# Performance work log

Hardware: AMD Instinct MI355X
Metric: run time of the kernel (lower is better)

## Reference

```python
import jax, jax.numpy as jnp
import numpy as np

D = 128  # hard-coded hidden dim in MLP_T

def setup_inputs() -> dict:
    key = jax.random.key(0)
    ks = jax.random.split(key, 8)
    N, IN = 16384, 768
    return {
        "x": jax.random.normal(ks[0], (N, IN), dtype=jnp.float32),
        "decay_value": 1,
        "W_token": jax.random.normal(ks[1], (IN, D), dtype=jnp.float32) * (IN ** -0.5),
        "b_token": jax.random.normal(ks[2], (D,), dtype=jnp.float32) * 0.02,
        "W_qkv": jax.random.normal(ks[3], (D, 3 * D), dtype=jnp.float32) * (D ** -0.5),
        "b_qkv": jax.random.normal(ks[4], (3 * D,), dtype=jnp.float32) * 0.02,
        "W_fc": jax.random.normal(ks[5], (D, 1), dtype=jnp.float32) * (D ** -0.5),
        "b_fc": jax.random.normal(ks[6], (1,), dtype=jnp.float32) * 0.02,
    }

def reference(x, decay_value, W_token, b_token, W_qkv, b_qkv, W_fc, b_fc):
    # token projection: [N, in_chan] -> [N, 128]
    h = x @ W_token + b_token
    # qkv: [N, 384] split along feature dim into q, k, v of [N, 128]
    qkv = h @ W_qkv + b_qkv
    q, k, v = qkv[:, :D], qkv[:, D:2 * D], qkv[:, 2 * D:]
    # sigmoid attention (no row normalization); dropout is identity in eval mode
    att_scores = jax.nn.sigmoid(q @ k.T)            # [N, N]
    att = att_scores @ v                            # [N, 128]
    out = att @ W_fc + b_fc                         # [N, 1]
    # GradientReversal is identity in the forward pass
    return out
```

## Files before the change

kernel.cpp:

```cpp
#include <hip/hip_runtime.h>
#include <hip/hip_bf16.h>
#include <stdint.h>

#define N_ROWS 16384

typedef __bf16 bf16x8 __attribute__((ext_vector_type(8)));
typedef float f32x4 __attribute__((ext_vector_type(4)));

#define AS1 __attribute__((address_space(1)))
#define AS3 __attribute__((address_space(3)))

#define OFF_WCS  0u
#define OFF_BC   589824u
#define OFF_QB   591360u
#define OFF_KB   4785664u
#define OFF_WV   8979968u
#define OFF_PART 9045504u

__global__ void prep(const float* __restrict__ Wt, const float* __restrict__ Wq,
                     const float* __restrict__ bt, const float* __restrict__ bq,
                     __bf16* __restrict__ WcS, float* __restrict__ bc) {
    int u = blockIdx.x * 256 + threadIdx.x;
    if (u < 768 * 96) {
        int k = u / 96, n4 = u % 96;
        float s[4] = {0, 0, 0, 0};
        const float* wtp = Wt + k * 128;
        const float* wqp = Wq + n4 * 4;
#pragma unroll 8
        for (int d = 0; d < 128; d++) {
            float a = wtp[d];
            float4 b = *(const float4*)(wqp + d * 384);
            s[0] += a * b.x; s[1] += a * b.y; s[2] += a * b.z; s[3] += a * b.w;
        }
        int kb_ = k >> 6, c = (k >> 3) & 7, k7 = k & 7;
#pragma unroll
        for (int j = 0; j < 4; j++) {
            int n = n4 * 4 + j;
            WcS[n * 768 + kb_ * 64 + ((c ^ (n & 7)) << 3) + k7] = (__bf16)s[j];
        }
    }
    if (u < 384) {
        float s = bq[u];
        for (int d = 0; d < 128; d++) s += bt[d] * Wq[d * 384 + u];
        bc[u] = s;
    }
}

__launch_bounds__(256)
__global__ void gemm_qkv(const float* __restrict__ x, const __bf16* __restrict__ WcS,
                         const float* __restrict__ bc, const float* __restrict__ W_fc,
                         __bf16* __restrict__ qb, __bf16* __restrict__ kb,
                         float* __restrict__ wv) {
    __shared__ float  Asm[64 * 64];
    __shared__ __bf16 Bsm[128 * 64];
    __shared__ float  wred[64];
    const int tid = threadIdx.x, wave = tid >> 6, lane = tid & 63;
    const int n16 = lane & 15, q = lane >> 4;
    const int mh = wave >> 1, nw = wave & 1;
    const int row0 = blockIdx.x * 64;
    const int sp = blockIdx.y;

    const char* aptr[4];
    const char* bptr[4];
    {
        int p = (lane & 15) >> 1, half = lane & 1;
#pragma unroll
        for (int i = 0; i < 4; i++) {
            int ar = row0 + wave * 16 + i * 4 + (lane >> 4);
            aptr[i] = (const char*)x + (size_t)ar * 3072 + ((p ^ (ar & 7)) * 8 + half * 4) * 4;
            int br = sp * 128 + wave * 32 + i * 8 + (lane >> 3);
            bptr[i] = (const char*)WcS + (size_t)br * 1536 + (lane & 7) * 16;
        }
    }
    f32x4 acc[2][4];
#pragma unroll
    for (int mt = 0; mt < 2; mt++)
#pragma unroll
        for (int t = 0; t < 4; t++) acc[mt][t] = (f32x4){0, 0, 0, 0};

    for (int kbi = 0; kbi < 12; kbi++) {
#pragma unroll
        for (int i = 0; i < 4; i++)
            __builtin_amdgcn_global_load_lds((const AS1 void*)(aptr[i] + kbi * 256),
                (AS3 void*)((char*)Asm + wave * 4096 + i * 1024), 16, 0, 0);
#pragma unroll
        for (int i = 0; i < 4; i++)
            __builtin_amdgcn_global_load_lds((const AS1 void*)(bptr[i] + kbi * 128),
                (AS3 void*)((char*)Bsm + wave * 4096 + i * 1024), 16, 0, 0);
        __syncthreads();
#pragma unroll
        for (int ks = 0; ks < 2; ks++) {
            const int swz = ((ks * 4 + q) ^ (n16 & 7)) << 3;
            bf16x8 af[2];
#pragma unroll
            for (int mt = 0; mt < 2; mt++) {
                const float* ap = Asm + (mh * 32 + mt * 16 + n16) * 64 + swz;
                f32x4 a0 = *(const f32x4*)ap;
                f32x4 a1 = *(const f32x4*)(ap + 4);
                bf16x8 t;
                t[0] = (__bf16)a0[0]; t[1] = (__bf16)a0[1]; t[2] = (__bf16)a0[2]; t[3] = (__bf16)a0[3];
                t[4] = (__bf16)a1[0]; t[5] = (__bf16)a1[1]; t[6] = (__bf16)a1[2]; t[7] = (__bf16)a1[3];
                af[mt] = t;
            }
#pragma unroll
            for (int t = 0; t < 4; t++) {
                bf16x8 bf = *(const bf16x8*)(Bsm + (nw * 64 + t * 16 + n16) * 64 + swz);
                acc[0][t] = __builtin_amdgcn_mfma_f32_16x16x32_bf16(af[0], bf, acc[0][t], 0, 0, 0);
                acc[1][t] = __builtin_amdgcn_mfma_f32_16x16x32_bf16(af[1], bf, acc[1][t], 0, 0, 0);
            }
        }
        __syncthreads();
    }

    const int clb = nw * 64 + n16;
    if (sp == 0) {
#pragma unroll
        for (int t = 0; t < 4; t++) {
            int cl = clb + t * 16;
            float bcv = bc[cl];
#pragma unroll
            for (int mt = 0; mt < 2; mt++)
#pragma unroll
                for (int r = 0; r < 4; r++) {
                    int row = row0 + mh * 32 + mt * 16 + q * 4 + r;
                    qb[row * 128 + cl] = (__bf16)((acc[mt][t][r] + bcv) * -1.44269504088896f);
                }
        }
    } else if (sp == 1) {
#pragma unroll
        for (int t = 0; t < 4; t++) {
            int d = clb + t * 16;
            float bcv = bc[128 + d];
#pragma unroll
            for (int mt = 0; mt < 2; mt++)
#pragma unroll
                for (int r = 0; r < 4; r++) {
                    int row = row0 + mh * 32 + mt * 16 + q * 4 + r;
                    kb[row * 128 + (((d >> 3) ^ (row & 15)) << 3) + (d & 7)] = (__bf16)(acc[mt][t][r] + bcv);
                }
        }
    } else {
        float wacc[2][4] = {{0, 0, 0, 0}, {0, 0, 0, 0}};
#pragma unroll
        for (int t = 0; t < 4; t++) {
            int cl = clb + t * 16;
            float bcv = bc[256 + cl];
            float wf = W_fc[cl];
#pragma unroll
            for (int mt = 0; mt < 2; mt++)
#pragma unroll
                for (int r = 0; r < 4; r++) wacc[mt][r] += (acc[mt][t][r] + bcv) * wf;
        }
        float vred[2][4];
#pragma unroll
        for (int mt = 0; mt < 2; mt++)
#pragma unroll
            for (int r = 0; r < 4; r++) {
                float v = wacc[mt][r];
                v += __shfl_xor(v, 1, 64);
                v += __shfl_xor(v, 2, 64);
                v += __shfl_xor(v, 4, 64);
                v += __shfl_xor(v, 8, 64);
                vred[mt][r] = v;
                if (nw == 0 && n16 == 0) wred[mh * 32 + mt * 16 + q * 4 + r] = v;
            }
        __syncthreads();
        if (nw == 1 && n16 == 0) {
#pragma unroll
            for (int mt = 0; mt < 2; mt++)
#pragma unroll
                for (int r = 0; r < 4; r++) {
                    int lr = mh * 32 + mt * 16 + q * 4 + r;
                    wv[row0 + lr] = wred[lr] + vred[mt][r];
                }
        }
    }
}

__launch_bounds__(256, 4)
__global__ void attn(const __bf16* __restrict__ qb, const __bf16* __restrict__ kb,
                     const float* __restrict__ wv, float* __restrict__ partial) {
    __shared__ __bf16 kbuf[4 * 32 * 128];
    const int tid = threadIdx.x;
    const int wave = tid >> 6, lane = tid & 63;
    const int n16 = lane & 15, q = lane >> 4;
    const int bid = blockIdx.x;
    const int sp = bid & 7;
    const int rb = bid >> 3;
    const int row0 = rb * 128 + wave * 32;
    const int jb0 = sp * 2048;

    bf16x8 qf[2][4];
#pragma unroll
    for (int mt = 0; mt < 2; mt++)
#pragma unroll
        for (int ks = 0; ks < 4; ks++)
            qf[mt][ks] = *(const bf16x8*)(qb + (size_t)(row0 + mt * 16 + n16) * 128 + ks * 32 + q * 8);

    float acc[2][4] = {{0}, {0}};

#define ISSUE(c, slot)                                                                  \
    {                                                                                   \
        const char* gsrc = (const char*)kb + (size_t)(jb0 + (c) * 32) * 256 + wave * 2048; \
        char* gdst = (char*)kbuf + (slot) * 8192 + wave * 2048;                          \
        __builtin_amdgcn_global_load_lds((const AS1 void*)(gsrc + lane * 16),            \
                                         (AS3 void*)gdst, 16, 0, 0);                     \
        __builtin_amdgcn_global_load_lds((const AS1 void*)(gsrc + 1024 + lane * 16),     \
                                         (AS3 void*)(gdst + 1024), 16, 0, 0);            \
    }

    ISSUE(0, 0);
    ISSUE(1, 1);

    for (int jc = 0; jc < 64; jc++) {
        const int jn = (jc + 2 < 64) ? jc + 2 : 63;
        ISSUE(jn, (jc + 2) & 3);

        asm volatile("s_waitcnt vmcnt(4)" ::: "memory");
        __builtin_amdgcn_sched_barrier(0);
        __builtin_amdgcn_s_barrier();

        const __bf16* curK = kbuf + (jc & 3) * 4096;
#pragma unroll
        for (int t = 0; t < 2; t++) {
            f32x4 s0 = (f32x4){0, 0, 0, 0}, s1 = (f32x4){0, 0, 0, 0};
#pragma unroll
            for (int ks = 0; ks < 4; ks++) {
                const int chunk = (ks * 4 + q) ^ n16;
                bf16x8 bf = *(const bf16x8*)(curK + (t * 16 + n16) * 128 + chunk * 8);
                s0 = __builtin_amdgcn_mfma_f32_16x16x32_bf16(qf[0][ks], bf, s0, 0, 0, 0);
                s1 = __builtin_amdgcn_mfma_f32_16x16x32_bf16(qf[1][ks], bf, s1, 0, 0, 0);
            }
            const float wval = wv[jb0 + jc * 32 + t * 16 + n16];
#pragma unroll
            for (int r = 0; r < 4; r++) {
                acc[0][r] += __builtin_amdgcn_rcpf(1.0f + __builtin_amdgcn_exp2f(s0[r])) * wval;
                acc[1][r] += __builtin_amdgcn_rcpf(1.0f + __builtin_amdgcn_exp2f(s1[r])) * wval;
            }
        }
    }
#undef ISSUE

#pragma unroll
    for (int mt = 0; mt < 2; mt++)
#pragma unroll
        for (int r = 0; r < 4; r++) {
            float v = acc[mt][r];
            v += __shfl_xor(v, 1, 64);
            v += __shfl_xor(v, 2, 64);
            v += __shfl_xor(v, 4, 64);
            v += __shfl_xor(v, 8, 64);
            if (n16 == 0) partial[sp * N_ROWS + row0 + mt * 16 + q * 4 + r] = v;
        }
}

__global__ void reduce_out(const float* __restrict__ partial, const float* __restrict__ b_fc,
                           float* __restrict__ out) {
    int i = blockIdx.x * 256 + threadIdx.x;
    float v = b_fc[0];
#pragma unroll
    for (int s = 0; s < 8; s++) v += partial[s * N_ROWS + i];
    out[i] = v;
}

extern "C" void kernel_launch(void* const* d_in, const int* in_sizes, int n_in,
                              void* d_out, int out_size, void* d_ws, size_t ws_size,
                              hipStream_t stream) {
    const float* x       = (const float*)d_in[0];
    const float* W_token = (const float*)d_in[2];
    const float* b_token = (const float*)d_in[3];
    const float* W_qkv   = (const float*)d_in[4];
    const float* b_qkv   = (const float*)d_in[5];
    const float* W_fc    = (const float*)d_in[6];
    const float* b_fc    = (const float*)d_in[7];
    float* out = (float*)d_out;
    char* ws = (char*)d_ws;

    __bf16* WcS = (__bf16*)(ws + OFF_WCS);
    float*  bc  = (float*)(ws + OFF_BC);
    __bf16* qb  = (__bf16*)(ws + OFF_QB);
    __bf16* kb  = (__bf16*)(ws + OFF_KB);
    float*  wv  = (float*)(ws + OFF_WV);
    float*  part = (float*)(ws + OFF_PART);

    prep<<<288, 256, 0, stream>>>(W_token, W_qkv, b_token, b_qkv, WcS, bc);
    gemm_qkv<<<dim3(256, 3), 256, 0, stream>>>(x, WcS, bc, W_fc, qb, kb, wv);
    attn<<<1024, 256, 0, stream>>>(qb, kb, wv, part);
    reduce_out<<<64, 256, 0, stream>>>(part, b_fc, out);
}
```

Measured before the change: 203.8 us.

## Software-pipeline sigmoid epilogue behind next MFMA tile and process K chunks in pairs

```diff
diff --git a/kernel.cpp b/kernel.cpp
--- a/kernel.cpp
+++ b/kernel.cpp
@@ -196,50 +196,76 @@
 #pragma unroll
         for (int ks = 0; ks < 4; ks++)
             qf[mt][ks] = *(const bf16x8*)(qb + (size_t)(row0 + mt * 16 + n16) * 128 + ks * 32 + q * 8);
-
-    float acc[2][4] = {{0}, {0}};
-
-#define ISSUE(c, slot)                                                                  \
-    {                                                                                   \
-        const char* gsrc = (const char*)kb + (size_t)(jb0 + (c) * 32) * 256 + wave * 2048; \
-        char* gdst = (char*)kbuf + (slot) * 8192 + wave * 2048;                          \
-        __builtin_amdgcn_global_load_lds((const AS1 void*)(gsrc + lane * 16),            \
-                                         (AS3 void*)gdst, 16, 0, 0);                     \
-        __builtin_amdgcn_global_load_lds((const AS1 void*)(gsrc + 1024 + lane * 16),     \
-                                         (AS3 void*)(gdst + 1024), 16, 0, 0);            \
-    }
+    __builtin_amdgcn_sched_barrier(0);
+
+    auto ISSUE = [&](int c, int slot) {
+        const char* gsrc = (const char*)kb + (size_t)(jb0 + c * 32) * 256 + wave * 2048;
+        char* gdst = (char*)kbuf + slot * 8192 + wave * 2048;
+        __builtin_amdgcn_global_load_lds((const AS1 void*)(gsrc + lane * 16),
+                                         (AS3 void*)gdst, 16, 0, 0);
+        __builtin_amdgcn_global_load_lds((const AS1 void*)(gsrc + 1024 + lane * 16),
+                                         (AS3 void*)(gdst + 1024), 16, 0, 0);
+    };
 
     ISSUE(0, 0);
     ISSUE(1, 1);
 
-    for (int jc = 0; jc < 64; jc++) {
-        const int jn = (jc + 2 < 64) ? jc + 2 : 63;
-        ISSUE(jn, (jc + 2) & 3);
-
-        asm volatile("s_waitcnt vmcnt(4)" ::: "memory");
+    float acc[2][4] = {{0}, {0}};
+    f32x4 ps0 = (f32x4){0, 0, 0, 0}, ps1 = (f32x4){0, 0, 0, 0};
+    float pw = 0.0f;
+
+    const __bf16* kaddr[4];
+#pragma unroll
+    for (int ks = 0; ks < 4; ks++)
+        kaddr[ks] = kbuf + n16 * 128 + (((ks * 4 + q) ^ n16) << 3);
+    const float* wsl = wv + jb0 + n16;
+
+    auto STEP = [&](int off, float wnew) {
+        f32x4 s0 = (f32x4){0, 0, 0, 0}, s1 = (f32x4){0, 0, 0, 0};
+        __builtin_amdgcn_s_setprio(1);
+#pragma unroll
+        for (int ks = 0; ks < 4; ks++) {
+            bf16x8 bf = *(const bf16x8*)(kaddr[ks] + off);
+            s0 = __builtin_amdgcn_mfma_f32_16x16x32_bf16(qf[0][ks], bf, s0, 0, 0, 0);
+            s1 = __builtin_amdgcn_mfma_f32_16x16x32_bf16(qf[1][ks], bf, s1, 0, 0, 0);
+        }
+        __builtin_amdgcn_s_setprio(0);
+#pragma unroll
+        for (int r = 0; r < 4; r++) {
+            acc[0][r] += __builtin_amdgcn_rcpf(1.0f + __builtin_amdgcn_exp2f(ps0[r])) * pw;
+            acc[1][r] += __builtin_amdgcn_rcpf(1.0f + __builtin_amdgcn_exp2f(ps1[r])) * pw;
+        }
+        ps0 = s0; ps1 = s1; pw = wnew;
+    };
+
+    auto PAIR = [&](int p, int sb) {
+        asm volatile("s_waitcnt vmcnt(0)" ::: "memory");
         __builtin_amdgcn_sched_barrier(0);
         __builtin_amdgcn_s_barrier();
-
-        const __bf16* curK = kbuf + (jc & 3) * 4096;
-#pragma unroll
-        for (int t = 0; t < 2; t++) {
-            f32x4 s0 = (f32x4){0, 0, 0, 0}, s1 = (f32x4){0, 0, 0, 0};
-#pragma unroll
-            for (int ks = 0; ks < 4; ks++) {
-                const int chunk = (ks * 4 + q) ^ n16;
-                bf16x8 bf = *(const bf16x8*)(curK + (t * 16 + n16) * 128 + chunk * 8);
-                s0 = __builtin_amdgcn_mfma_f32_16x16x32_bf16(qf[0][ks], bf, s0, 0, 0, 0);
-                s1 = __builtin_amdgcn_mfma_f32_16x16x32_bf16(qf[1][ks], bf, s1, 0, 0, 0);
-            }
-            const float wval = wv[jb0 + jc * 32 + t * 16 + n16];
-#pragma unroll
-            for (int r = 0; r < 4; r++) {
-                acc[0][r] += __builtin_amdgcn_rcpf(1.0f + __builtin_amdgcn_exp2f(s0[r])) * wval;
-                acc[1][r] += __builtin_amdgcn_rcpf(1.0f + __builtin_amdgcn_exp2f(s1[r])) * wval;
-            }
-        }
-    }
-#undef ISSUE
+        const int c2 = (2 * p + 2 < 64) ? 2 * p + 2 : 62;
+        const int c3 = (2 * p + 3 < 64) ? 2 * p + 3 : 63;
+        ISSUE(c2, sb ^ 2);
+        ISSUE(c3, (sb ^ 2) + 1);
+        float w0 = wsl[p * 64];
+        float w1 = wsl[p * 64 + 16];
+        float w2 = wsl[p * 64 + 32];
+        float w3 = wsl[p * 64 + 48];
+        STEP(sb * 4096,        w0);
+        STEP(sb * 4096 + 2048, w1);
+        STEP(sb * 4096 + 4096, w2);
+        STEP(sb * 4096 + 6144, w3);
+    };
+
+    for (int p = 0; p < 32; p += 2) {
+        PAIR(p, 0);
+        PAIR(p + 1, 2);
+    }
+
+#pragma unroll
+    for (int r = 0; r < 4; r++) {
+        acc[0][r] += __builtin_amdgcn_rcpf(1.0f + __builtin_amdgcn_exp2f(ps0[r])) * pw;
+        acc[1][r] += __builtin_amdgcn_rcpf(1.0f + __builtin_amdgcn_exp2f(ps1[r])) * pw;
+    }
 
 #pragma unroll
     for (int mt = 0; mt < 2; mt++)
```

New measurement: 234.4 us. 15.0% more time.

## Software-pipeline sigmoid epilogue against next tile's MFMAs in attention loop

Applied to the files above, without the earlier changes.

```diff
diff --git a/kernel.cpp b/kernel.cpp
--- a/kernel.cpp
+++ b/kernel.cpp
@@ -196,8 +196,7 @@
 #pragma unroll
         for (int ks = 0; ks < 4; ks++)
             qf[mt][ks] = *(const bf16x8*)(qb + (size_t)(row0 + mt * 16 + n16) * 128 + ks * 32 + q * 8);
-
-    float acc[2][4] = {{0}, {0}};
+    __builtin_amdgcn_sched_barrier(0);
 
 #define ISSUE(c, slot)                                                                  \
     {                                                                                   \
@@ -209,37 +208,73 @@
                                          (AS3 void*)(gdst + 1024), 16, 0, 0);            \
     }
 
+    const float* wsl = wv + jb0 + n16;
+    float wnA0 = wsl[0], wnA1 = wsl[16];
+    float wnB0 = 0.0f, wnB1 = 0.0f;
+    __builtin_amdgcn_sched_barrier(0);
     ISSUE(0, 0);
     ISSUE(1, 1);
 
+    float acc[2][4] = {{0}, {0}};
+    f32x4 psE0 = (f32x4){0, 0, 0, 0}, psE1 = (f32x4){0, 0, 0, 0};
+    f32x4 psO0 = (f32x4){0, 0, 0, 0}, psO1 = (f32x4){0, 0, 0, 0};
+    float pw = 0.0f;
+
+    const __bf16* kaddr[4];
+#pragma unroll
+    for (int ks = 0; ks < 4; ks++)
+        kaddr[ks] = kbuf + n16 * 128 + (((ks * 4 + q) ^ n16) << 3);
+
+#define STEP(SW0, SW1, SR0, SR1, OFFB, WCUR)                                            \
+    {                                                                                   \
+        SW0 = (f32x4){0, 0, 0, 0};                                                      \
+        SW1 = (f32x4){0, 0, 0, 0};                                                      \
+        __builtin_amdgcn_s_setprio(1);                                                  \
+        _Pragma("unroll")                                                               \
+        for (int ks = 0; ks < 4; ks++) {                                                \
+            bf16x8 bf = *(const bf16x8*)(kaddr[ks] + (OFFB));                           \
+            SW0 = __builtin_amdgcn_mfma_f32_16x16x32_bf16(qf[0][ks], bf, SW0, 0, 0, 0); \
+            SW1 = __builtin_amdgcn_mfma_f32_16x16x32_bf16(qf[1][ks], bf, SW1, 0, 0, 0); \
+        }                                                                               \
+        __builtin_amdgcn_s_setprio(0);                                                  \
+        _Pragma("unroll")                                                               \
+        for (int r = 0; r < 4; r++) {                                                   \
+            acc[0][r] += __builtin_amdgcn_rcpf(1.0f + __builtin_amdgcn_exp2f(SR0[r])) * pw; \
+            acc[1][r] += __builtin_amdgcn_rcpf(1.0f + __builtin_amdgcn_exp2f(SR1[r])) * pw; \
+        }                                                                               \
+        pw = (WCUR);                                                                    \
+    }
+
+#pragma unroll 4
     for (int jc = 0; jc < 64; jc++) {
-        const int jn = (jc + 2 < 64) ? jc + 2 : 63;
-        ISSUE(jn, (jc + 2) & 3);
-
+        const int jn1 = (jc + 1 < 64) ? jc + 1 : 63;
+        if (((jc + 1) & 1) == 0) { wnA0 = wsl[jn1 * 32]; wnA1 = wsl[jn1 * 32 + 16]; }
+        else                     { wnB0 = wsl[jn1 * 32]; wnB1 = wsl[jn1 * 32 + 16]; }
+        __builtin_amdgcn_sched_barrier(0);
+        const int jn2 = (jc + 2 < 64) ? jc + 2 : 62;
+        ISSUE(jn2, (jc + 2) & 3);
+        __builtin_amdgcn_sched_barrier(0);
         asm volatile("s_waitcnt vmcnt(4)" ::: "memory");
         __builtin_amdgcn_sched_barrier(0);
         __builtin_amdgcn_s_barrier();
 
-        const __bf16* curK = kbuf + (jc & 3) * 4096;
-#pragma unroll
-        for (int t = 0; t < 2; t++) {
-            f32x4 s0 = (f32x4){0, 0, 0, 0}, s1 = (f32x4){0, 0, 0, 0};
-#pragma unroll
-            for (int ks = 0; ks < 4; ks++) {
-                const int chunk = (ks * 4 + q) ^ n16;
-                bf16x8 bf = *(const bf16x8*)(curK + (t * 16 + n16) * 128 + chunk * 8);
-                s0 = __builtin_amdgcn_mfma_f32_16x16x32_bf16(qf[0][ks], bf, s0, 0, 0, 0);
-                s1 = __builtin_amdgcn_mfma_f32_16x16x32_bf16(qf[1][ks], bf, s1, 0, 0, 0);
-            }
-            const float wval = wv[jb0 + jc * 32 + t * 16 + n16];
-#pragma unroll
-            for (int r = 0; r < 4; r++) {
-                acc[0][r] += __builtin_amdgcn_rcpf(1.0f + __builtin_amdgcn_exp2f(s0[r])) * wval;
-                acc[1][r] += __builtin_amdgcn_rcpf(1.0f + __builtin_amdgcn_exp2f(s1[r])) * wval;
-            }
-        }
-    }
+        const int sb = (jc & 3) * 4096;
+        if ((jc & 1) == 0) {
+            STEP(psE0, psE1, psO0, psO1, sb, wnA0);
+            STEP(psO0, psO1, psE0, psE1, sb + 2048, wnA1);
+        } else {
+            STEP(psE0, psE1, psO0, psO1, sb, wnB0);
+            STEP(psO0, psO1, psE0, psE1, sb + 2048, wnB1);
+        }
+    }
+#undef STEP
 #undef ISSUE
+
+#pragma unroll
+    for (int r = 0; r < 4; r++) {
+        acc[0][r] += __builtin_amdgcn_rcpf(1.0f + __builtin_amdgcn_exp2f(psO0[r])) * pw;
+        acc[1][r] += __builtin_amdgcn_rcpf(1.0f + __builtin_amdgcn_exp2f(psO1[r])) * pw;
+    }
 
 #pragma unroll
     for (int mt = 0; mt < 2; mt++)
```

Result: no change. 204.0 us (+0.1%).

## Load K directly into registers and software-pipeline MFMA with sigmoid

Applied to the files above, without the earlier changes.

```diff
diff --git a/kernel.cpp b/kernel.cpp
--- a/kernel.cpp
+++ b/kernel.cpp
@@ -136,7 +136,7 @@
 #pragma unroll
                 for (int r = 0; r < 4; r++) {
                     int row = row0 + mh * 32 + mt * 16 + q * 4 + r;
-                    kb[row * 128 + (((d >> 3) ^ (row & 15)) << 3) + (d & 7)] = (__bf16)(acc[mt][t][r] + bcv);
+                    kb[row * 128 + d] = (__bf16)(acc[mt][t][r] + bcv);
                 }
         }
     } else {
@@ -180,7 +180,6 @@
 __launch_bounds__(256, 4)
 __global__ void attn(const __bf16* __restrict__ qb, const __bf16* __restrict__ kb,
                      const float* __restrict__ wv, float* __restrict__ partial) {
-    __shared__ __bf16 kbuf[4 * 32 * 128];
     const int tid = threadIdx.x;
     const int wave = tid >> 6, lane = tid & 63;
     const int n16 = lane & 15, q = lane >> 4;
@@ -197,49 +196,67 @@
         for (int ks = 0; ks < 4; ks++)
             qf[mt][ks] = *(const bf16x8*)(qb + (size_t)(row0 + mt * 16 + n16) * 128 + ks * 32 + q * 8);
 
+    const char* kp = (const char*)kb + (size_t)(jb0 + n16) * 256 + q * 16;
+    const float* wq = wv + jb0 + n16;
+
+    bf16x8 bfA[4], bfB[4];
+#pragma unroll
+    for (int ks = 0; ks < 4; ks++) bfA[ks] = *(const bf16x8*)(kp + ks * 64);
+
+    f32x4 psA0 = (f32x4){0,0,0,0}, psA1 = (f32x4){0,0,0,0};
+    f32x4 psB0 = (f32x4){0,0,0,0}, psB1 = (f32x4){0,0,0,0};
+    float wA = 0.0f, wB = 0.0f;
     float acc[2][4] = {{0}, {0}};
 
-#define ISSUE(c, slot)                                                                  \
+#define MFMA8(P0, P1, BF)                                                               \
     {                                                                                   \
-        const char* gsrc = (const char*)kb + (size_t)(jb0 + (c) * 32) * 256 + wave * 2048; \
-        char* gdst = (char*)kbuf + (slot) * 8192 + wave * 2048;                          \
-        __builtin_amdgcn_global_load_lds((const AS1 void*)(gsrc + lane * 16),            \
-                                         (AS3 void*)gdst, 16, 0, 0);                     \
-        __builtin_amdgcn_global_load_lds((const AS1 void*)(gsrc + 1024 + lane * 16),     \
-                                         (AS3 void*)(gdst + 1024), 16, 0, 0);            \
-    }
-
-    ISSUE(0, 0);
-    ISSUE(1, 1);
-
-    for (int jc = 0; jc < 64; jc++) {
-        const int jn = (jc + 2 < 64) ? jc + 2 : 63;
-        ISSUE(jn, (jc + 2) & 3);
-
-        asm volatile("s_waitcnt vmcnt(4)" ::: "memory");
-        __builtin_amdgcn_sched_barrier(0);
-        __builtin_amdgcn_s_barrier();
-
-        const __bf16* curK = kbuf + (jc & 3) * 4096;
-#pragma unroll
-        for (int t = 0; t < 2; t++) {
-            f32x4 s0 = (f32x4){0, 0, 0, 0}, s1 = (f32x4){0, 0, 0, 0};
-#pragma unroll
-            for (int ks = 0; ks < 4; ks++) {
-                const int chunk = (ks * 4 + q) ^ n16;
-                bf16x8 bf = *(const bf16x8*)(curK + (t * 16 + n16) * 128 + chunk * 8);
-                s0 = __builtin_amdgcn_mfma_f32_16x16x32_bf16(qf[0][ks], bf, s0, 0, 0, 0);
-                s1 = __builtin_amdgcn_mfma_f32_16x16x32_bf16(qf[1][ks], bf, s1, 0, 0, 0);
-            }
-            const float wval = wv[jb0 + jc * 32 + t * 16 + n16];
-#pragma unroll
-            for (int r = 0; r < 4; r++) {
-                acc[0][r] += __builtin_amdgcn_rcpf(1.0f + __builtin_amdgcn_exp2f(s0[r])) * wval;
-                acc[1][r] += __builtin_amdgcn_rcpf(1.0f + __builtin_amdgcn_exp2f(s1[r])) * wval;
-            }
-        }
-    }
-#undef ISSUE
+        P0 = (f32x4){0,0,0,0}; P1 = (f32x4){0,0,0,0};                                   \
+        __builtin_amdgcn_s_setprio(1);                                                  \
+        _Pragma("unroll")                                                               \
+        for (int ks = 0; ks < 4; ks++) {                                                \
+            P0 = __builtin_amdgcn_mfma_f32_16x16x32_bf16(qf[0][ks], BF[ks], P0, 0, 0, 0); \
+            P1 = __builtin_amdgcn_mfma_f32_16x16x32_bf16(qf[1][ks], BF[ks], P1, 0, 0, 0); \
+        }                                                                               \
+        __builtin_amdgcn_s_setprio(0);                                                  \
+    }
+#define SIG(R0, R1, W)                                                                  \
+    {                                                                                   \
+        _Pragma("unroll")                                                               \
+        for (int r = 0; r < 4; r++) {                                                   \
+            acc[0][r] += __builtin_amdgcn_rcpf(1.0f + __builtin_amdgcn_exp2f(R0[r])) * (W); \
+            acc[1][r] += __builtin_amdgcn_rcpf(1.0f + __builtin_amdgcn_exp2f(R1[r])) * (W); \
+        }                                                                               \
+    }
+
+    for (int t2 = 0; t2 < 64; t2++) {
+        kp += 4096;
+        {
+            bf16x8 n0 = *(const bf16x8*)(kp);
+            bf16x8 n1 = *(const bf16x8*)(kp + 64);
+            bf16x8 n2 = *(const bf16x8*)(kp + 128);
+            bf16x8 n3 = *(const bf16x8*)(kp + 192);
+            float wa = *wq; wq += 16;
+            MFMA8(psA0, psA1, bfA);
+            SIG(psB0, psB1, wB);
+            bfB[0] = n0; bfB[1] = n1; bfB[2] = n2; bfB[3] = n3;
+            wA = wa;
+        }
+        kp += 4096;
+        {
+            bf16x8 n0 = *(const bf16x8*)(kp);
+            bf16x8 n1 = *(const bf16x8*)(kp + 64);
+            bf16x8 n2 = *(const bf16x8*)(kp + 128);
+            bf16x8 n3 = *(const bf16x8*)(kp + 192);
+            float wb = *wq; wq += 16;
+            MFMA8(psB0, psB1, bfB);
+            SIG(psA0, psA1, wA);
+            bfA[0] = n0; bfA[1] = n1; bfA[2] = n2; bfA[3] = n3;
+            wB = wb;
+        }
+    }
+    SIG(psB0, psB1, wB);
+#undef MFMA8
+#undef SIG
 
 #pragma unroll
     for (int mt = 0; mt < 2; mt++)
```

Result: slower. 356.9 us (+75.1%).
